# Kernel optimization log

Hardware: AMD Instinct MI355X
Metric: run time of the kernel (lower is better)

Reference implementation:

```python
import jax, jax.numpy as jnp
import numpy as np

N_CB, VOCAB, CDIM = 8, 1024, 16
DECAY = 0.99
EPS = 1e-5


def setup_inputs() -> dict:
    key = jax.random.key(0)
    k1, k2, k3 = jax.random.split(key, 3)
    z = jax.random.normal(k1, (8, N_CB * CDIM, 32, 32), jnp.float32)
    codebooks = jax.random.normal(k2, (N_CB, VOCAB, CDIM), jnp.float32) * 0.02
    ema_count = jnp.zeros((N_CB, VOCAB), jnp.float32)
    ema_weight = jax.random.normal(k3, (N_CB, VOCAB, CDIM), jnp.float32) * 0.02
    return {"z": z, "codebooks": codebooks, "ema_count": ema_count, "ema_weight": ema_weight}


def reference(z, codebooks, ema_count, ema_weight):
    B, D, H, W = z.shape
    # (b d h w) -> (b h w, n_cb, cdim): matches rearrange + chunk(dim=-1)
    zp = z.transpose(0, 2, 3, 1).reshape(B * H * W, N_CB, CDIM)
    # squared distances (N, C, V): |z|^2 - 2 z.cb + |cb|^2
    d2 = (jnp.sum(zp * zp, axis=-1, keepdims=True)
          - 2.0 * jnp.einsum('ncd,cvd->ncv', zp, codebooks)
          + jnp.sum(codebooks * codebooks, axis=-1)[None, :, :])
    idx = jnp.argmin(d2, axis=-1)                      # (N, C) int
    zq = codebooks[jnp.arange(N_CB)[None, :], idx]     # (N, C, d) gather

    # --- EMA codebook update (training-mode math, no grad) ---
    idx_c = idx.T                                      # (C, N)
    zp_c = zp.transpose(1, 0, 2)                       # (C, N, d)
    counts = jax.vmap(lambda i: jnp.zeros((VOCAB,), jnp.float32).at[i].add(1.0))(idx_c)
    sums = jax.vmap(lambda i, x: jnp.zeros((VOCAB, CDIM), jnp.float32).at[i].add(x))(idx_c, zp_c)
    new_count = DECAY * ema_count + (1.0 - DECAY) * counts
    new_weight = DECAY * ema_weight + (1.0 - DECAY) * sums
    n = jnp.sum(new_count, axis=-1, keepdims=True)     # (C, 1)
    count = (new_count + EPS) / (n + VOCAB * EPS) * n  # Laplace-smoothed counts
    new_codebooks = new_weight / count[..., None]

    # commitment: mean over codebooks of per-part MSE == global MSE (equal part sizes)
    commitment = jnp.mean((zp - jax.lax.stop_gradient(zq)) ** 2)

    # straight-through estimator
    zq_st = zp + jax.lax.stop_gradient(zq - zp)        # (N, C, d)
    quantized = zq_st.reshape(B, H, W, D).transpose(0, 3, 1, 2)
    indices = idx.reshape(B, H, W, N_CB).transpose(0, 3, 1, 2)  # (B, C, H, W)
    return quantized, indices, commitment, new_codebooks, new_count, new_weight
```

## Files before the change

### kernel.cpp

```cpp
#include <hip/hip_runtime.h>


#define NCB   8
#define VOCAB 1024
#define CDIM  16
#define NPIX  8192
#define HW    1024

#define OFF_QUANT  0
#define OFF_IDX    1048576
#define OFF_COMMIT 1114112
#define OFF_NCB    1114113
#define OFF_NCNT   1245185
#define OFF_NWT    1253377

#define WS_CNTP_OFF 0
#define WS_SUMP_OFF (NCB * 2 * VOCAB)
#define WS_CARR_OFF (NCB * 2 * VOCAB + NCB * CDIM * 2 * VOCAB)

__device__ __forceinline__ float npsum16(const float m[16]) {
#pragma clang fp contract(off)
  float r0 = m[0] + m[8];
  float r1 = m[1] + m[9];
  float r2 = m[2] + m[10];
  float r3 = m[3] + m[11];
  float r4 = m[4] + m[12];
  float r5 = m[5] + m[13];
  float r6 = m[6] + m[14];
  float r7 = m[7] + m[15];
  return ((r0 + r1) + (r2 + r3)) + ((r4 + r5) + (r6 + r7));
}

__device__ __forceinline__ float npsum16sq(const float a[16]) {
#pragma clang fp contract(off)
  float m[16];
#pragma unroll
  for (int d = 0; d < 16; ++d) m[d] = a[d] * a[d];
  return npsum16(m);
}

__device__ __forceinline__ void proc_entry(const float zv[16],
                                           const float e[16], float c2v,
                                           float z2, int idx, float& best,
                                           int& bi) {
#pragma clang fp contract(off)
  float m[16];
#pragma unroll
  for (int d = 0; d < 16; ++d) m[d] = zv[d] * e[d];
  float l0 = (m[0] + m[4]) + (m[8] + m[12]);
  float l1 = (m[1] + m[5]) + (m[9] + m[13]);
  float l2 = (m[2] + m[6]) + (m[10] + m[14]);
  float l3 = (m[3] + m[7]) + (m[11] + m[15]);
  const float dot = (l0 + l1) + (l2 + l3);
  const float d2 = (z2 - 2.0f * dot) + c2v;
  const bool lt = d2 < best;
  best = lt ? d2 : best;
  bi = lt ? idx : bi;
}

__global__ __launch_bounds__(512, 4) void k_assign(
    const float* __restrict__ z, const float* __restrict__ cb,
    float* __restrict__ out, float* __restrict__ ws_commit_arr) {
  __shared__ float s_c2[VOCAB];
  __shared__ float s_best[8 * 64];
  __shared__ int s_bi[8 * 64];

  const int c = blockIdx.x >> 7;
  const int pchunk = blockIdx.x & 127;
  const int t = threadIdx.x;
  const int pix = t & 63;
  const int w = t >> 6;
  const int wu = __builtin_amdgcn_readfirstlane(w);

  const float* cbc = cb + (size_t)c * VOCAB * CDIM;

  for (int v = t; v < VOCAB; v += 512) {
    float e[16];
#pragma unroll
    for (int d = 0; d < 16; ++d) e[d] = cbc[(size_t)v * CDIM + d];
    s_c2[v] = npsum16sq(e);
  }

  const int n = pchunk * 64 + pix;
  const int b = n >> 10;
  const int hw = n & 1023;

  const float* zbase = z + ((size_t)(b * 128 + c * 16)) * HW + hw;
  float zv[16];
#pragma unroll
  for (int d = 0; d < 16; ++d) zv[d] = zbase[(size_t)d * HW];

  const float z2 = npsum16sq(zv);

  __syncthreads();

  const int vbase = wu * 128;
  const float* ep = cbc + (size_t)vbase * CDIM;

  float best = INFINITY;
  int bi = 0;

#pragma unroll 2
  for (int k = 0; k < 128; k += 2) {
    float ea[16], eb[16];
#pragma unroll
    for (int d = 0; d < 16; ++d) ea[d] = ep[(size_t)k * CDIM + d];
#pragma unroll
    for (int d = 0; d < 16; ++d) eb[d] = ep[(size_t)(k + 1) * CDIM + d];
    const float cv0 = s_c2[vbase + k];
    const float cv1 = s_c2[vbase + k + 1];
    proc_entry(zv, ea, cv0, z2, vbase + k, best, bi);
    proc_entry(zv, eb, cv1, z2, vbase + k + 1, best, bi);
  }

  s_best[w * 64 + pix] = best;
  s_bi[w * 64 + pix] = bi;
  __syncthreads();

  if (t < 64) {
    best = s_best[t];
    bi = s_bi[t];
#pragma unroll
    for (int s = 1; s < 8; ++s) {
      const float ob = s_best[s * 64 + t];
      const int oi = s_bi[s * 64 + t];
      const bool take = (ob < best) || (ob == best && oi < bi);
      best = take ? ob : best;
      bi = take ? oi : bi;
    }

    const float* qe = cbc + (size_t)bi * CDIM;
    float comm = 0.f;
#pragma unroll
    for (int d = 0; d < 16; ++d) {
      float zq = qe[d];
      float diff, qst;
      {
#pragma clang fp contract(off)
        diff = zv[d] - zq;
        qst = zv[d] + (zq - zv[d]);
      }
      comm += diff * diff;
      out[OFF_QUANT + ((size_t)(b * 128 + c * 16 + d)) * HW + hw] = qst;
    }
    out[OFF_IDX + ((size_t)(b * NCB + c)) * HW + hw] = (float)bi;

#pragma unroll
    for (int off = 32; off; off >>= 1) comm += __shfl_down(comm, off);
    if (t == 0) atomicAdd(ws_commit_arr + blockIdx.x, 0.0f),
        ws_commit_arr[blockIdx.x] = comm;
  }
}

__global__ __launch_bounds__(1024, 4) void k_stats(
    const float* __restrict__ z, const float* __restrict__ outbuf,
    float* __restrict__ ws_counts_p, float* __restrict__ ws_sums_p) {
  __shared__ float s_sum[VOCAB];
  __shared__ float s_cnt[VOCAB];
  const int c = blockIdx.x >> 5;
  const int d = (blockIdx.x >> 1) & 15;
  const int half = blockIdx.x & 1;
  const int t = threadIdx.x;

  s_sum[t] = 0.f;
  if (d == 0) s_cnt[t] = 0.f;

  int bidx[4];
  float zval[4];
#pragma unroll
  for (int k = 0; k < 4; ++k) {
    const int bb = half * 4 + k;
    bidx[k] = (int)outbuf[OFF_IDX + ((size_t)(bb * NCB + c)) * HW + t];
    zval[k] = z[((size_t)(bb * 128 + c * 16 + d)) * HW + t];
  }
  __syncthreads();

#pragma unroll
  for (int k = 0; k < 4; ++k) {
    atomicAdd(&s_sum[bidx[k]], zval[k]);
    if (d == 0) atomicAdd(&s_cnt[bidx[k]], 1.0f);
  }
  __syncthreads();

  ws_sums_p[((size_t)((c * CDIM + d) * 2 + half)) * VOCAB + t] = s_sum[t];
  if (d == 0) ws_counts_p[(c * 2 + half) * VOCAB + t] = s_cnt[t];
}

__global__ __launch_bounds__(256) void k_update(
    const float* __restrict__ ema_count, const float* __restrict__ ema_weight,
    const float* __restrict__ ws_counts_p, const float* __restrict__ ws_sums_p,
    const float* __restrict__ ws_commit_arr, float* __restrict__ out) {
  const int c = blockIdx.x >> 3;
  const int part = blockIdx.x & 7;
  const int t = threadIdx.x;
  __shared__ float s_red[4];
  __shared__ float s_n;
  __shared__ double s_dred[4];

  const float* cp0 = ws_counts_p + (c * 2 + 0) * VOCAB;
  const float* cp1 = ws_counts_p + (c * 2 + 1) * VOCAB;

  float psum = 0.f;
#pragma unroll
  for (int k = 0; k < 4; ++k) {
    const int v = k * 256 + t;
    psum += 0.99f * ema_count[c * VOCAB + v] + 0.01f * (cp0[v] + cp1[v]);
  }
#pragma unroll
  for (int off = 32; off; off >>= 1) psum += __shfl_down(psum, off);
  if ((t & 63) == 0) s_red[t >> 6] = psum;
  __syncthreads();
  if (t == 0) s_n = (s_red[0] + s_red[1]) + (s_red[2] + s_red[3]);
  __syncthreads();
  const float nsum = s_n;
  const float veps = 0.01024f;

  if (t < 128) {
    const int v = part * 128 + t;
    out[OFF_NCNT + c * VOCAB + v] =
        0.99f * ema_count[c * VOCAB + v] + 0.01f * (cp0[v] + cp1[v]);
  }

#pragma unroll
  for (int k = 0; k < 8; ++k) {
    const int i = part * 2048 + k * 256 + t;
    const int v = i >> 4;
    const int d = i & 15;
    const float nc =
        0.99f * ema_count[c * VOCAB + v] + 0.01f * (cp0[v] + cp1[v]);
    const float cnt = (nc + 1e-5f) / (nsum + veps) * nsum;
    const size_t gi = (size_t)c * VOCAB * CDIM + i;
    const float s0 = ws_sums_p[((size_t)((c * CDIM + d) * 2 + 0)) * VOCAB + v];
    const float s1 = ws_sums_p[((size_t)((c * CDIM + d) * 2 + 1)) * VOCAB + v];
    const float nw = 0.99f * ema_weight[gi] + 0.01f * (s0 + s1);
    out[OFF_NWT + gi] = nw;
    out[OFF_NCB + gi] = nw / cnt;
  }

  if (blockIdx.x == 0) {
    double ps = 0.0;
#pragma unroll
    for (int k = 0; k < 4; ++k) ps += (double)ws_commit_arr[k * 256 + t];
#pragma unroll
    for (int off = 32; off; off >>= 1) ps += __shfl_down(ps, off);
    if ((t & 63) == 0) s_dred[t >> 6] = ps;
    __syncthreads();
    if (t == 0)
      out[OFF_COMMIT] =
          (float)(((s_dred[0] + s_dred[1]) + (s_dred[2] + s_dred[3])) /
                  1048576.0);
  }
}

extern "C" void kernel_launch(void* const* d_in, const int* in_sizes, int n_in,
                              void* d_out, int out_size, void* d_ws,
                              size_t ws_size, hipStream_t stream) {
  const float* z = (const float*)d_in[0];
  const float* codebooks = (const float*)d_in[1];
  const float* ema_count = (const float*)d_in[2];
  const float* ema_weight = (const float*)d_in[3];
  float* out = (float*)d_out;

  float* wsf = (float*)d_ws;
  float* ws_counts_p = wsf + WS_CNTP_OFF;
  float* ws_sums_p = wsf + WS_SUMP_OFF;
  float* ws_commit_arr = wsf + WS_CARR_OFF;


  k_assign<<<dim3(1024), dim3(512), 0, stream>>>(z, codebooks, out,
                                                 ws_commit_arr);
  k_stats<<<dim3(256), dim3(1024), 0, stream>>>(z, out, ws_counts_p,
                                                ws_sums_p);
  k_update<<<dim3(64), dim3(256), 0, stream>>>(ema_count, ema_weight,
                                               ws_counts_p, ws_sums_p,
                                               ws_commit_arr, out);
}
```

Before: 133.8 us.

## Fuse EMA update into stats kernel via last-block-per-codebook counter

Removes the separate k_update launch by having each k_stats block increment a per-codebook atomic counter, with the last of the 32 blocks for a codebook performing that codebook's EMA count/weight/codebook update and, for codebook 0, the commitment reduction. Counters are reset inside k_assign. The dummy atomicAdd before the commitment store is also dropped. This saves one kernel launch and its gap, but the update work now runs on only 8 blocks instead of 64, which lowers parallelism for that phase and serializes it behind the slowest stats block.

```diff
diff --git a/kernel.cpp b/kernel.cpp
--- a/kernel.cpp
+++ b/kernel.cpp
@@ -17,6 +17,7 @@
 #define WS_CNTP_OFF 0
 #define WS_SUMP_OFF (NCB * 2 * VOCAB)
 #define WS_CARR_OFF (NCB * 2 * VOCAB + NCB * CDIM * 2 * VOCAB)
+#define WS_CTR_OFF  (WS_CARR_OFF + 1024)
 
 __device__ __forceinline__ float npsum16(const float m[16]) {
 #pragma clang fp contract(off)
@@ -60,7 +61,8 @@
 
 __global__ __launch_bounds__(512, 4) void k_assign(
     const float* __restrict__ z, const float* __restrict__ cb,
-    float* __restrict__ out, float* __restrict__ ws_commit_arr) {
+    float* __restrict__ out, float* __restrict__ ws_commit_arr,
+    unsigned int* __restrict__ ws_ctr) {
   __shared__ float s_c2[VOCAB];
   __shared__ float s_best[8 * 64];
   __shared__ int s_bi[8 * 64];
@@ -72,6 +74,8 @@
   const int w = t >> 6;
   const int wu = __builtin_amdgcn_readfirstlane(w);
 
+  if (blockIdx.x == 0 && t < NCB) ws_ctr[t] = 0u;
+
   const float* cbc = cb + (size_t)c * VOCAB * CDIM;
 
   for (int v = t; v < VOCAB; v += 512) {
@@ -147,16 +151,23 @@
 
 #pragma unroll
     for (int off = 32; off; off >>= 1) comm += __shfl_down(comm, off);
-    if (t == 0) atomicAdd(ws_commit_arr + blockIdx.x, 0.0f),
-        ws_commit_arr[blockIdx.x] = comm;
+    if (t == 0) ws_commit_arr[blockIdx.x] = comm;
   }
 }
 
 __global__ __launch_bounds__(1024, 4) void k_stats(
     const float* __restrict__ z, const float* __restrict__ outbuf,
-    float* __restrict__ ws_counts_p, float* __restrict__ ws_sums_p) {
+    const float* __restrict__ ema_count, const float* __restrict__ ema_weight,
+    float* __restrict__ ws_counts_p, float* __restrict__ ws_sums_p,
+    const float* __restrict__ ws_commit_arr, unsigned int* __restrict__ ws_ctr,
+    float* __restrict__ out) {
   __shared__ float s_sum[VOCAB];
   __shared__ float s_cnt[VOCAB];
+  __shared__ float s_red[4];
+  __shared__ float s_n;
+  __shared__ double s_dred[4];
+  __shared__ int s_last;
+
   const int c = blockIdx.x >> 5;
   const int d = (blockIdx.x >> 1) & 15;
   const int half = blockIdx.x & 1;
@@ -184,66 +195,62 @@
 
   ws_sums_p[((size_t)((c * CDIM + d) * 2 + half)) * VOCAB + t] = s_sum[t];
   if (d == 0) ws_counts_p[(c * 2 + half) * VOCAB + t] = s_cnt[t];
-}
-
-__global__ __launch_bounds__(256) void k_update(
-    const float* __restrict__ ema_count, const float* __restrict__ ema_weight,
-    const float* __restrict__ ws_counts_p, const float* __restrict__ ws_sums_p,
-    const float* __restrict__ ws_commit_arr, float* __restrict__ out) {
-  const int c = blockIdx.x >> 3;
-  const int part = blockIdx.x & 7;
-  const int t = threadIdx.x;
-  __shared__ float s_red[4];
-  __shared__ float s_n;
-  __shared__ double s_dred[4];
+
+  __threadfence();
+  if (t == 0) s_last = (atomicAdd(&ws_ctr[c], 1u) == 31u);
+  __syncthreads();
+  if (!s_last) return;
+  __threadfence();
 
   const float* cp0 = ws_counts_p + (c * 2 + 0) * VOCAB;
   const float* cp1 = ws_counts_p + (c * 2 + 1) * VOCAB;
 
-  float psum = 0.f;
-#pragma unroll
-  for (int k = 0; k < 4; ++k) {
-    const int v = k * 256 + t;
-    psum += 0.99f * ema_count[c * VOCAB + v] + 0.01f * (cp0[v] + cp1[v]);
-  }
-#pragma unroll
-  for (int off = 32; off; off >>= 1) psum += __shfl_down(psum, off);
-  if ((t & 63) == 0) s_red[t >> 6] = psum;
+  if (t < 256) {
+    float psum = 0.f;
+#pragma unroll
+    for (int k = 0; k < 4; ++k) {
+      const int v = k * 256 + t;
+      psum +=
+          0.99f * ema_count[c * VOCAB + v] + 0.01f * (cp0[v] + cp1[v]);
+    }
+#pragma unroll
+    for (int off = 32; off; off >>= 1) psum += __shfl_down(psum, off);
+    if ((t & 63) == 0) s_red[t >> 6] = psum;
+  }
   __syncthreads();
   if (t == 0) s_n = (s_red[0] + s_red[1]) + (s_red[2] + s_red[3]);
   __syncthreads();
   const float nsum = s_n;
   const float veps = 0.01024f;
 
-  if (t < 128) {
-    const int v = part * 128 + t;
-    out[OFF_NCNT + c * VOCAB + v] =
-        0.99f * ema_count[c * VOCAB + v] + 0.01f * (cp0[v] + cp1[v]);
-  }
-
-#pragma unroll
-  for (int k = 0; k < 8; ++k) {
-    const int i = part * 2048 + k * 256 + t;
+  out[OFF_NCNT + c * VOCAB + t] =
+      0.99f * ema_count[c * VOCAB + t] + 0.01f * (cp0[t] + cp1[t]);
+
+#pragma unroll
+  for (int j = 0; j < 16; ++j) {
+    const int i = j * 1024 + t;
     const int v = i >> 4;
-    const int d = i & 15;
+    const int dd = i & 15;
     const float nc =
         0.99f * ema_count[c * VOCAB + v] + 0.01f * (cp0[v] + cp1[v]);
     const float cnt = (nc + 1e-5f) / (nsum + veps) * nsum;
     const size_t gi = (size_t)c * VOCAB * CDIM + i;
-    const float s0 = ws_sums_p[((size_t)((c * CDIM + d) * 2 + 0)) * VOCAB + v];
-    const float s1 = ws_sums_p[((size_t)((c * CDIM + d) * 2 + 1)) * VOCAB + v];
+    const float s0 = ws_sums_p[((size_t)((c * CDIM + dd) * 2 + 0)) * VOCAB + v];
+    const float s1 = ws_sums_p[((size_t)((c * CDIM + dd) * 2 + 1)) * VOCAB + v];
     const float nw = 0.99f * ema_weight[gi] + 0.01f * (s0 + s1);
     out[OFF_NWT + gi] = nw;
     out[OFF_NCB + gi] = nw / cnt;
   }
 
-  if (blockIdx.x == 0) {
-    double ps = 0.0;
-#pragma unroll
-    for (int k = 0; k < 4; ++k) ps += (double)ws_commit_arr[k * 256 + t];
-#pragma unroll
-    for (int off = 32; off; off >>= 1) ps += __shfl_down(ps, off);
-    if ((t & 63) == 0) s_dred[t >> 6] = ps;
+  if (c == 0) {
+    if (t < 256) {
+      double ps = 0.0;
+#pragma unroll
+      for (int k = 0; k < 4; ++k) ps += (double)ws_commit_arr[k * 256 + t];
+#pragma unroll
+      for (int off = 32; off; off >>= 1) ps += __shfl_down(ps, off);
+      if ((t & 63) == 0) s_dred[t >> 6] = ps;
+    }
     __syncthreads();
     if (t == 0)
       out[OFF_COMMIT] =
@@ -265,13 +272,12 @@
   float* ws_counts_p = wsf + WS_CNTP_OFF;
   float* ws_sums_p = wsf + WS_SUMP_OFF;
   float* ws_commit_arr = wsf + WS_CARR_OFF;
+  unsigned int* ws_ctr = (unsigned int*)(wsf + WS_CTR_OFF);
 
 
   k_assign<<<dim3(1024), dim3(512), 0, stream>>>(z, codebooks, out,
-                                                 ws_commit_arr);
-  k_stats<<<dim3(256), dim3(1024), 0, stream>>>(z, out, ws_counts_p,
-                                                ws_sums_p);
-  k_update<<<dim3(64), dim3(256), 0, stream>>>(ema_count, ema_weight,
-                                               ws_counts_p, ws_sums_p,
-                                               ws_commit_arr, out);
-}
+                                                 ws_commit_arr, ws_ctr);
+  k_stats<<<dim3(256), dim3(1024), 0, stream>>>(z, out, ema_count, ema_weight,
+                                                ws_counts_p, ws_sums_p,
+                                                ws_commit_arr, ws_ctr, out);
+}
```

Result: slower. 216.5 us (+61.8%).

## Stage codebook in LDS and use packed fp32 math for distance search

Applied to the files above, without the earlier changes.

Each k_assign block now copies its codebook slice (64KB) into shared memory and reads entries from LDS as float4, where before it loaded wave-uniform values from global memory. The dot products are rewritten with 2-wide float vectors so the compiler can emit packed FP32 multiply/add, with the summation order changed. A dummy atomicAdd before the commit store is also removed. The 64KB LDS allocation limits blocks per CU, and the new summation order may change argmin tie behaviour.

```diff
diff --git a/kernel.cpp b/kernel.cpp
--- a/kernel.cpp
+++ b/kernel.cpp
@@ -17,6 +17,8 @@
 #define WS_CNTP_OFF 0
 #define WS_SUMP_OFF (NCB * 2 * VOCAB)
 #define WS_CARR_OFF (NCB * 2 * VOCAB + NCB * CDIM * 2 * VOCAB)
+
+typedef __attribute__((ext_vector_type(2))) float f32x2;
 
 __device__ __forceinline__ float npsum16(const float m[16]) {
 #pragma clang fp contract(off)
@@ -39,19 +41,22 @@
   return npsum16(m);
 }
 
-__device__ __forceinline__ void proc_entry(const float zv[16],
-                                           const float e[16], float c2v,
-                                           float z2, int idx, float& best,
-                                           int& bi) {
-#pragma clang fp contract(off)
-  float m[16];
-#pragma unroll
-  for (int d = 0; d < 16; ++d) m[d] = zv[d] * e[d];
-  float l0 = (m[0] + m[4]) + (m[8] + m[12]);
-  float l1 = (m[1] + m[5]) + (m[9] + m[13]);
-  float l2 = (m[2] + m[6]) + (m[10] + m[14]);
-  float l3 = (m[3] + m[7]) + (m[11] + m[15]);
-  const float dot = (l0 + l1) + (l2 + l3);
+__device__ __forceinline__ void proc_entry_pk(const f32x2 zp[8], float4 q0,
+                                              float4 q1, float4 q2, float4 q3,
+                                              float c2v, float z2, int idx,
+                                              float& best, int& bi) {
+#pragma clang fp contract(off)
+  f32x2 e[8];
+  e[0] = f32x2{q0.x, q0.y}; e[1] = f32x2{q0.z, q0.w};
+  e[2] = f32x2{q1.x, q1.y}; e[3] = f32x2{q1.z, q1.w};
+  e[4] = f32x2{q2.x, q2.y}; e[5] = f32x2{q2.z, q2.w};
+  e[6] = f32x2{q3.x, q3.y}; e[7] = f32x2{q3.z, q3.w};
+  f32x2 m[8];
+#pragma unroll
+  for (int j = 0; j < 8; ++j) m[j] = zp[j] * e[j];
+  const f32x2 l01 = (m[0] + m[2]) + (m[4] + m[6]);
+  const f32x2 l23 = (m[1] + m[3]) + (m[5] + m[7]);
+  const float dot = (l01.x + l01.y) + (l23.x + l23.y);
   const float d2 = (z2 - 2.0f * dot) + c2v;
   const bool lt = d2 < best;
   best = lt ? d2 : best;
@@ -61,6 +66,7 @@
 __global__ __launch_bounds__(512, 4) void k_assign(
     const float* __restrict__ z, const float* __restrict__ cb,
     float* __restrict__ out, float* __restrict__ ws_commit_arr) {
+  __shared__ float s_cb[VOCAB * CDIM];
   __shared__ float s_c2[VOCAB];
   __shared__ float s_best[8 * 64];
   __shared__ int s_bi[8 * 64];
@@ -73,6 +79,11 @@
   const int wu = __builtin_amdgcn_readfirstlane(w);
 
   const float* cbc = cb + (size_t)c * VOCAB * CDIM;
+  const float4* cb4 = reinterpret_cast<const float4*>(cbc);
+  float4* s_cb4 = reinterpret_cast<float4*>(s_cb);
+
+#pragma unroll
+  for (int i = 0; i < 8; ++i) s_cb4[i * 512 + t] = cb4[i * 512 + t];
 
   for (int v = t; v < VOCAB; v += 512) {
     float e[16];
@@ -92,25 +103,28 @@
 
   const float z2 = npsum16sq(zv);
 
+  f32x2 zp[8];
+#pragma unroll
+  for (int j = 0; j < 8; ++j) zp[j] = f32x2{zv[2 * j], zv[2 * j + 1]};
+
   __syncthreads();
 
   const int vbase = wu * 128;
-  const float* ep = cbc + (size_t)vbase * CDIM;
+  const float4* sl4 = s_cb4 + (size_t)vbase * 4;
 
   float best = INFINITY;
   int bi = 0;
 
 #pragma unroll 2
   for (int k = 0; k < 128; k += 2) {
-    float ea[16], eb[16];
-#pragma unroll
-    for (int d = 0; d < 16; ++d) ea[d] = ep[(size_t)k * CDIM + d];
-#pragma unroll
-    for (int d = 0; d < 16; ++d) eb[d] = ep[(size_t)(k + 1) * CDIM + d];
+    const float4 a0 = sl4[k * 4 + 0], a1 = sl4[k * 4 + 1];
+    const float4 a2 = sl4[k * 4 + 2], a3 = sl4[k * 4 + 3];
+    const float4 b0 = sl4[k * 4 + 4], b1 = sl4[k * 4 + 5];
+    const float4 b2 = sl4[k * 4 + 6], b3 = sl4[k * 4 + 7];
     const float cv0 = s_c2[vbase + k];
     const float cv1 = s_c2[vbase + k + 1];
-    proc_entry(zv, ea, cv0, z2, vbase + k, best, bi);
-    proc_entry(zv, eb, cv1, z2, vbase + k + 1, best, bi);
+    proc_entry_pk(zp, a0, a1, a2, a3, cv0, z2, vbase + k, best, bi);
+    proc_entry_pk(zp, b0, b1, b2, b3, cv1, z2, vbase + k + 1, best, bi);
   }
 
   s_best[w * 64 + pix] = best;
@@ -147,8 +161,7 @@
 
 #pragma unroll
     for (int off = 32; off; off >>= 1) comm += __shfl_down(comm, off);
-    if (t == 0) atomicAdd(ws_commit_arr + blockIdx.x, 0.0f),
-        ws_commit_arr[blockIdx.x] = comm;
+    if (t == 0) ws_commit_arr[blockIdx.x] = comm;
   }
 }
 
```

Result: no change. 134.4 us (+0.5%).
